# Kernel optimization log

Hardware: AMD Instinct MI355X
Metric: run time of the kernel (lower is better)

Reference implementation:

```python
import jax, jax.numpy as jnp
import numpy as np

N, IN_F, OUT_F, K = 256, 8192, 8320, 16
J = OUT_F - IN_F  # 128


def setup_inputs() -> dict:
    key = jax.random.key(0)
    k1, k2 = jax.random.split(key)
    tensor = jax.random.normal(k1, (N, IN_F), dtype=jnp.float32)
    T = jax.random.normal(k2, (IN_F, J, K), dtype=jnp.float32)
    return {"tensor": tensor, "T": T}


def reference(tensor, T):
    # flatten(start_dim=1) is identity for rank-2 input
    x = tensor.reshape(tensor.shape[0], -1)            # [N, IN_F]
    feats = jnp.einsum('ni,ijk->njk', x, T)            # [N, J, K]
    # pairwise L1 across batch: [N,1,J,K] - [N,J,K] -> [N,N,J,K]
    diff = jnp.abs(feats[:, None, :, :] - feats[None, :, :, :])
    l1 = jnp.sum(diff, axis=3)                         # [N, N, J]
    diversity = jnp.sum(jnp.exp(-l1), axis=1)          # [N, J]
    return jnp.concatenate((x, diversity), axis=1)     # [N, IN_F + J]
```

## Files before the change

### kernel.cpp

```cpp
#include <hip/hip_runtime.h>

typedef unsigned int  u32;
typedef unsigned short u16;

typedef __bf16 bf16x8 __attribute__((ext_vector_type(8)));
typedef float  floatx4 __attribute__((ext_vector_type(4)));

#define N_ROWS 256
#define IN_F   8192
#define OUT_F  8320
#define JDIM   128
#define KDIM   16
#define JK     2048

#define BM     256
#define BN     64
#define BK     64
#define WSTRIDE 72

#define SLAB_U16   (N_ROWS * JK)
#define JSLICE_U16 (N_ROWS * KDIM)

typedef const __attribute__((address_space(1))) u32 gu32;
typedef __attribute__((address_space(3))) u32 su32;

__device__ __forceinline__ u16 f2bf(float f) {
    u32 u = __float_as_uint(f);
    return (u16)((u + 0x7fffu + ((u >> 16) & 1u)) >> 16);
}
__device__ __forceinline__ float bf2f(u16 h) { return __uint_as_float(((u32)h) << 16); }

__device__ __forceinline__ u32 cvtpk(float lo, float hi) {
    u32 d;
    asm("v_cvt_pk_bf16_f32 %0, %1, %2" : "=v"(d) : "v"(lo), "v"(hi));
    return d;
}

template<int S>
__global__ __launch_bounds__(256, 2) void gemm_kernel(const float* __restrict__ X,
                                                      const float* __restrict__ W,
                                                      u16* __restrict__ slabs,
                                                      float* __restrict__ out)
{
    constexpr int KCH   = IN_F / S;
    constexpr int ITERS = KCH >> 6;

    __shared__ __align__(16) float xsf[BM * BK];
    __shared__ __align__(16) u16   wt[BN * WSTRIDE];

    const int tid  = threadIdx.x;
    const int lane = tid & 63;
    const int wave = tid >> 6;

    int xblk, s;
    {
        int lin = blockIdx.x;
        if constexpr (S == 16) {
            int rem = lin >> 3;
            xblk = rem & 31;
            s = ((lin & 7) << 1) | (rem >> 5);
        } else if constexpr (S == 8) {
            s = lin & 7; xblk = lin >> 3;
        } else {
            xblk = lin & 31; s = lin >> 5;
        }
    }
    const int c0     = xblk * BN;
    const int k0base = s * KCH;

    if (s == 0) {
        int g = xblk * 256 + tid;
        int r2 = g >> 5, j4 = g & 31;
        reinterpret_cast<float4*>(out + (size_t)r2 * OUT_F + IN_F)[j4] =
            make_float4(0.f, 0.f, 0.f, 0.f);
    }

    floatx4 acc[4][4] = {};

    const int row_in = lane >> 4;
    const int slot   = lane & 15;

    const int wk = (tid >> 4) << 2;
    const int wc = (tid & 15) << 2;
    const float* wptr = W + (size_t)(k0base + wk) * JK + c0 + wc;

    float4 wreg[4];
    #pragma unroll
    for (int r = 0; r < 4; ++r)
        wreg[r] = *(const float4*)(wptr + (size_t)r * JK);

    for (int it = 0; it < ITERS; ++it) {
        const int k0 = k0base + it * BK;
        __syncthreads();

        #pragma unroll
        for (int g = 0; g < 16; ++g) {
            int rbase = wave * 64 + g * 4;
            int gch   = slot ^ (4 * (g & 3) + row_in);
            const float* gp = X + (size_t)(rbase + row_in) * IN_F + k0 + gch * 4;
            u32* lp = (u32*)&xsf[rbase * BK];
            __builtin_amdgcn_global_load_lds((gu32*)gp, (su32*)lp, 16, 0, 0);
        }

        {
            const float* wr = (const float*)wreg;
            #pragma unroll
            for (int i = 0; i < 4; ++i) {
                uint2 v;
                v.x = cvtpk(wr[0 * 4 + i], wr[1 * 4 + i]);
                v.y = cvtpk(wr[2 * 4 + i], wr[3 * 4 + i]);
                *(uint2*)&wt[(wc + i) * WSTRIDE + wk] = v;
            }
        }
        __syncthreads();

        if (it + 1 < ITERS) {
            const float* wn = wptr + (size_t)(it + 1) * BK * JK;
            #pragma unroll
            for (int r = 0; r < 4; ++r)
                wreg[r] = *(const float4*)(wn + (size_t)r * JK);
        }

        const int mrow = lane & 15;
        const int q    = lane >> 4;
        #pragma unroll
        for (int h = 0; h < 2; ++h) {
            bf16x8 a[4], b[4];
            #pragma unroll
            for (int rt = 0; rt < 4; ++rt) {
                int rl = wave * 64 + rt * 16 + mrow;
                int t2 = (h * 4 + q) * 2;
                int s0 = t2 ^ mrow;
                int s1 = s0 ^ 1;
                float4 u0 = *(const float4*)&xsf[rl * BK + s0 * 4];
                float4 u1 = *(const float4*)&xsf[rl * BK + s1 * 4];
                union { u32 u[4]; bf16x8 v; } pk;
                pk.u[0] = cvtpk(u0.x, u0.y);
                pk.u[1] = cvtpk(u0.z, u0.w);
                pk.u[2] = cvtpk(u1.x, u1.y);
                pk.u[3] = cvtpk(u1.z, u1.w);
                a[rt] = pk.v;
            }
            #pragma unroll
            for (int ct = 0; ct < 4; ++ct) {
                int col = ct * 16 + mrow;
                b[ct] = *reinterpret_cast<const bf16x8*>(&wt[col * WSTRIDE + (h * 4 + q) * 8]);
            }
            #pragma unroll
            for (int rt = 0; rt < 4; ++rt)
                #pragma unroll
                for (int ct = 0; ct < 4; ++ct)
                    acc[rt][ct] = __builtin_amdgcn_mfma_f32_16x16x32_bf16(a[rt], b[ct], acc[rt][ct], 0, 0, 0);
        }
    }

    const int qe = lane >> 4;
    const int cl = lane & 15;
    u16* sp = slabs + (size_t)s * SLAB_U16;
    #pragma unroll
    for (int rt = 0; rt < 4; ++rt)
        #pragma unroll
        for (int ct = 0; ct < 4; ++ct) {
            int j = (c0 >> 4) + ct;
            #pragma unroll
            for (int r = 0; r < 4; ++r) {
                int row = wave * 64 + rt * 16 + qe * 4 + r;
                sp[(size_t)j * JSLICE_U16 + row * KDIM + cl] = f2bf(acc[rt][ct][r]);
            }
        }
}

template<int S>
__global__ __launch_bounds__(256) void fused_rp_kernel(const u16* __restrict__ slabs,
                                                       const float* __restrict__ X,
                                                       float* __restrict__ out)
{
    const int j  = blockIdx.x;
    const int mq = blockIdx.y;
    const int n  = threadIdx.x;
    const int lin = blockIdx.y * JDIM + blockIdx.x;
    const int g0  = lin * 256 + n;

    __shared__ float F[N_ROWS * KDIM];

    const u16* base = slabs + (size_t)j * JSLICE_U16 + n * KDIM;

    float f[16];
    #pragma unroll
    for (int k = 0; k < 16; ++k) f[k] = 0.f;

    #pragma unroll
    for (int so = 0; so < S; so += 4) {
        uint4 va[4], vb[4];
        #pragma unroll
        for (int i = 0; i < 4 && so + i < S; ++i) {
            const u16* p = base + (size_t)(so + i) * SLAB_U16;
            va[i] = *(const uint4*)p;
            vb[i] = *(const uint4*)(p + 8);
        }
        #pragma unroll
        for (int i = 0; i < 4 && so + i < S; ++i) {
            const u16* ha = (const u16*)&va[i];
            const u16* hb = (const u16*)&vb[i];
            #pragma unroll
            for (int e = 0; e < 8; ++e) {
                f[e]     += bf2f(ha[e]);
                f[8 + e] += bf2f(hb[e]);
            }
        }
    }

    float4* Fp = (float4*)&F[n * KDIM];
    Fp[0] = make_float4(f[0],  f[1],  f[2],  f[3]);
    Fp[1] = make_float4(f[4],  f[5],  f[6],  f[7]);
    Fp[2] = make_float4(f[8],  f[9],  f[10], f[11]);
    Fp[3] = make_float4(f[12], f[13], f[14], f[15]);

    float4 cp[4];
    #pragma unroll
    for (int i = 0; i < 4; ++i)
        cp[i] = reinterpret_cast<const float4*>(X)[g0 + i * 131072];

    __syncthreads();

    float accum = 0.f;
    const int m0 = mq * 64;
    #pragma unroll 2
    for (int m = 0; m < 64; ++m) {
        const float* Fm = &F[(m0 + m) * KDIM];
        float l1 = 0.f;
        #pragma unroll
        for (int k = 0; k < 16; ++k) l1 += fabsf(f[k] - Fm[k]);
        accum += exp2f(-1.4426950408889634f * l1);
    }
    atomicAdd(&out[(size_t)n * OUT_F + IN_F + j], accum);

    #pragma unroll
    for (int i = 0; i < 4; ++i) {
        int t = g0 + i * 131072;
        int row = t >> 11, c4 = t & 2047;
        reinterpret_cast<float4*>(out + (size_t)row * OUT_F)[c4] = cp[i];
    }
}

extern "C" void kernel_launch(void* const* d_in, const int* in_sizes, int n_in,
                              void* d_out, int out_size, void* d_ws, size_t ws_size,
                              hipStream_t stream)
{
    const float* X = (const float*)d_in[0];
    const float* T = (const float*)d_in[1];
    float* out = (float*)d_out;

    u16* slabs = (u16*)d_ws;

    int S = 16;
    if (ws_size < (size_t)16 * SLAB_U16 * 2) S = 8;
    if (ws_size < (size_t)8  * SLAB_U16 * 2) S = 4;

    if (S == 16) {
        gemm_kernel<16><<<512, 256, 0, stream>>>(X, T, slabs, out);
        fused_rp_kernel<16><<<dim3(JDIM, 4), 256, 0, stream>>>(slabs, X, out);
    } else if (S == 8) {
        gemm_kernel<8><<<256, 256, 0, stream>>>(X, T, slabs, out);
        fused_rp_kernel<8><<<dim3(JDIM, 4), 256, 0, stream>>>(slabs, X, out);
    } else {
        gemm_kernel<4><<<128, 256, 0, stream>>>(X, T, slabs, out);
        fused_rp_kernel<4><<<dim3(JDIM, 4), 256, 0, stream>>>(slabs, X, out);
    }
}
```

Baseline: 142.3 us.

## Pre-convert X to bf16 in a prep kernel and stage bf16 tiles in LDS

Adds a prep kernel that converts the fp32 activations X to bf16 into the workspace. The GEMM then loads bf16 tiles directly into LDS with a new XOR swizzle, which halves LDS footprint and global traffic for X and removes the per-iteration fp32-to-bf16 packing on the A operand. The inline-asm packed convert for W is also replaced with software rounding. The cost is an extra kernel launch plus an extra read and write pass over X, and the workspace is split to hold Xb.

```diff
diff --git a/kernel.cpp b/kernel.cpp
--- a/kernel.cpp
+++ b/kernel.cpp
@@ -30,14 +30,18 @@
 }
 __device__ __forceinline__ float bf2f(u16 h) { return __uint_as_float(((u32)h) << 16); }
 
-__device__ __forceinline__ u32 cvtpk(float lo, float hi) {
-    u32 d;
-    asm("v_cvt_pk_bf16_f32 %0, %1, %2" : "=v"(d) : "v"(lo), "v"(hi));
-    return d;
+__global__ __launch_bounds__(256) void prep_kernel(const float* __restrict__ X,
+                                                   u16* __restrict__ Xb)
+{
+    int t = blockIdx.x * 256 + threadIdx.x;
+    float4 v = reinterpret_cast<const float4*>(X)[t];
+    ushort4 b;
+    b.x = f2bf(v.x); b.y = f2bf(v.y); b.z = f2bf(v.z); b.w = f2bf(v.w);
+    reinterpret_cast<ushort4*>(Xb)[t] = b;
 }
 
 template<int S>
-__global__ __launch_bounds__(256, 2) void gemm_kernel(const float* __restrict__ X,
+__global__ __launch_bounds__(256, 2) void gemm_kernel(const u16* __restrict__ Xb,
                                                       const float* __restrict__ W,
                                                       u16* __restrict__ slabs,
                                                       float* __restrict__ out)
@@ -45,8 +49,8 @@
     constexpr int KCH   = IN_F / S;
     constexpr int ITERS = KCH >> 6;
 
-    __shared__ __align__(16) float xsf[BM * BK];
-    __shared__ __align__(16) u16   wt[BN * WSTRIDE];
+    __shared__ __align__(16) u16 xs[BM * BK];
+    __shared__ __align__(16) u16 wt[BN * WSTRIDE];
 
     const int tid  = threadIdx.x;
     const int lane = tid & 63;
@@ -77,11 +81,11 @@
 
     floatx4 acc[4][4] = {};
 
-    const int row_in = lane >> 4;
-    const int slot   = lane & 15;
-
-    const int wk = (tid >> 4) << 2;
-    const int wc = (tid & 15) << 2;
+    const int xrl = lane >> 3;
+    const int xgc = (lane & 7) ^ xrl;
+    const int wk  = (tid >> 4) << 2;
+    const int wc  = (tid & 15) << 2;
+
     const float* wptr = W + (size_t)(k0base + wk) * JK + c0 + wc;
 
     float4 wreg[4];
@@ -94,11 +98,10 @@
         __syncthreads();
 
         #pragma unroll
-        for (int g = 0; g < 16; ++g) {
-            int rbase = wave * 64 + g * 4;
-            int gch   = slot ^ (4 * (g & 3) + row_in);
-            const float* gp = X + (size_t)(rbase + row_in) * IN_F + k0 + gch * 4;
-            u32* lp = (u32*)&xsf[rbase * BK];
+        for (int g = 0; g < 8; ++g) {
+            int rbase = wave * 64 + g * 8;
+            const u16* gp = Xb + (size_t)(rbase + xrl) * IN_F + k0 + xgc * 8;
+            u32* lp = (u32*)&xs[rbase * BK];
             __builtin_amdgcn_global_load_lds((gu32*)gp, (su32*)lp, 16, 0, 0);
         }
 
@@ -106,9 +109,9 @@
             const float* wr = (const float*)wreg;
             #pragma unroll
             for (int i = 0; i < 4; ++i) {
-                uint2 v;
-                v.x = cvtpk(wr[0 * 4 + i], wr[1 * 4 + i]);
-                v.y = cvtpk(wr[2 * 4 + i], wr[3 * 4 + i]);
+                u32 lo = (u32)f2bf(wr[0 * 4 + i]) | ((u32)f2bf(wr[1 * 4 + i]) << 16);
+                u32 hi = (u32)f2bf(wr[2 * 4 + i]) | ((u32)f2bf(wr[3 * 4 + i]) << 16);
+                uint2 v; v.x = lo; v.y = hi;
                 *(uint2*)&wt[(wc + i) * WSTRIDE + wk] = v;
             }
         }
@@ -128,18 +131,9 @@
             bf16x8 a[4], b[4];
             #pragma unroll
             for (int rt = 0; rt < 4; ++rt) {
-                int rl = wave * 64 + rt * 16 + mrow;
-                int t2 = (h * 4 + q) * 2;
-                int s0 = t2 ^ mrow;
-                int s1 = s0 ^ 1;
-                float4 u0 = *(const float4*)&xsf[rl * BK + s0 * 4];
-                float4 u1 = *(const float4*)&xsf[rl * BK + s1 * 4];
-                union { u32 u[4]; bf16x8 v; } pk;
-                pk.u[0] = cvtpk(u0.x, u0.y);
-                pk.u[1] = cvtpk(u0.z, u0.w);
-                pk.u[2] = cvtpk(u1.x, u1.y);
-                pk.u[3] = cvtpk(u1.z, u1.w);
-                a[rt] = pk.v;
+                int rl   = wave * 64 + rt * 16 + mrow;
+                int slot = (h * 4 + q) ^ (rl & 7);
+                a[rt] = *reinterpret_cast<const bf16x8*>(&xs[rl * BK + slot * 8]);
             }
             #pragma unroll
             for (int ct = 0; ct < 4; ++ct) {
@@ -251,20 +245,22 @@
     const float* T = (const float*)d_in[1];
     float* out = (float*)d_out;
 
-    u16* slabs = (u16*)d_ws;
+    u16* Xb    = (u16*)d_ws;
+    u16* slabs = (u16*)((char*)d_ws + (4u << 20));
 
     int S = 16;
-    if (ws_size < (size_t)16 * SLAB_U16 * 2) S = 8;
-    if (ws_size < (size_t)8  * SLAB_U16 * 2) S = 4;
-
+    if (ws_size < (4u << 20) + (size_t)16 * SLAB_U16 * 2) S = 8;
+    if (ws_size < (4u << 20) + (size_t)8  * SLAB_U16 * 2) S = 4;
+
+    prep_kernel<<<2048, 256, 0, stream>>>(X, Xb);
     if (S == 16) {
-        gemm_kernel<16><<<512, 256, 0, stream>>>(X, T, slabs, out);
+        gemm_kernel<16><<<512, 256, 0, stream>>>(Xb, T, slabs, out);
         fused_rp_kernel<16><<<dim3(JDIM, 4), 256, 0, stream>>>(slabs, X, out);
     } else if (S == 8) {
-        gemm_kernel<8><<<256, 256, 0, stream>>>(X, T, slabs, out);
+        gemm_kernel<8><<<256, 256, 0, stream>>>(Xb, T, slabs, out);
         fused_rp_kernel<8><<<dim3(JDIM, 4), 256, 0, stream>>>(slabs, X, out);
     } else {
-        gemm_kernel<4><<<128, 256, 0, stream>>>(X, T, slabs, out);
+        gemm_kernel<4><<<128, 256, 0, stream>>>(Xb, T, slabs, out);
         fused_rp_kernel<4><<<dim3(JDIM, 4), 256, 0, stream>>>(slabs, X, out);
     }
 }
```

After: 141.9 us. Within noise of the previous version (-0.3%).
